# Optimization experiments

Measured on AMD Instinct MI355X. Metric: run time of the kernel, lower is better.

## Reference

```python
import jax, jax.numpy as jnp
import numpy as np

N_NODES = 50000
N_EDGES = 800000
NEG_SLOPE = 0.2  # DGL GATConv default LeakyReLU slope


def _gat_layer(h, src, dst, W, attn_l, attn_r, bias, activation):
    """One DGL-style GATConv (eval mode, no dropout).
    h: [N, Din]; W: [Din, H*F]; attn_l/attn_r: [H, F]; bias: [H*F].
    Returns [N, H, F].
    """
    H, F = attn_l.shape
    feat = (h @ W).reshape(-1, H, F)                      # [N, H, F]
    el = jnp.sum(feat * attn_l[None], axis=-1)            # [N, H]
    er = jnp.sum(feat * attn_r[None], axis=-1)            # [N, H]
    e = jax.nn.leaky_relu(el[src] + er[dst], NEG_SLOPE)   # [E, H]
    # segment softmax over incoming edges of each dst node
    m = jax.ops.segment_max(e, dst, num_segments=N_NODES)  # [N, H]
    ex = jnp.exp(e - m[dst])                               # [E, H]
    s = jax.ops.segment_sum(ex, dst, num_segments=N_NODES)  # [N, H]
    alpha = ex / s[dst]                                    # [E, H]
    msg = feat[src] * alpha[..., None]                     # [E, H, F]
    out = jax.ops.segment_sum(msg, dst, num_segments=N_NODES)  # [N, H, F]
    out = out + bias.reshape(1, H, F)
    if activation is not None:
        out = activation(out)
    return out


def setup_inputs() -> dict:
    key = jax.random.key(0)
    ks = jax.random.split(key, 16)
    in_size, hid, h0, h2, out_size = 256, 16, 8, 1, 64
    d1 = hid * h0  # 128
    inp = {
        "x": jax.random.normal(ks[0], (N_NODES, in_size), dtype=jnp.float32),
        "src": jax.random.randint(ks[1], (N_EDGES,), 0, N_NODES, dtype=jnp.int32),
        "dst": jax.random.randint(ks[2], (N_EDGES,), 0, N_NODES, dtype=jnp.int32),
        "W0": jax.random.normal(ks[3], (in_size, h0 * hid), dtype=jnp.float32) * 0.1,
        "al0": jax.random.normal(ks[4], (h0, hid), dtype=jnp.float32) * 0.1,
        "ar0": jax.random.normal(ks[5], (h0, hid), dtype=jnp.float32) * 0.1,
        "b0": jnp.zeros((h0 * hid,), dtype=jnp.float32),
        "W1": jax.random.normal(ks[6], (d1, h0 * hid), dtype=jnp.float32) * 0.1,
        "al1": jax.random.normal(ks[7], (h0, hid), dtype=jnp.float32) * 0.1,
        "ar1": jax.random.normal(ks[8], (h0, hid), dtype=jnp.float32) * 0.1,
        "b1": jnp.zeros((h0 * hid,), dtype=jnp.float32),
        "W2": jax.random.normal(ks[9], (d1, h2 * out_size), dtype=jnp.float32) * 0.1,
        "al2": jax.random.normal(ks[10], (h2, out_size), dtype=jnp.float32) * 0.1,
        "ar2": jax.random.normal(ks[11], (h2, out_size), dtype=jnp.float32) * 0.1,
        "b2": jnp.zeros((h2 * out_size,), dtype=jnp.float32),
    }
    return inp


def reference(x, src, dst, W0, al0, ar0, b0, W1, al1, ar1, b1, W2, al2, ar2, b2):
    elu = jax.nn.elu
    h = _gat_layer(x, src, dst, W0, al0, ar0, b0, elu)      # [N, 8, 16]
    h = h.reshape(h.shape[0], -1)                           # flatten heads -> [N, 128]
    h = _gat_layer(h, src, dst, W1, al1, ar1, b1, elu)      # [N, 8, 16]
    h = h.reshape(h.shape[0], -1)                           # [N, 128]
    h = _gat_layer(h, src, dst, W2, al2, ar2, b2, None)     # [N, 1, 64]
    return h.mean(axis=1)                                   # [N, 64]
```

## Files before the change

### kernel.cpp

```cpp
#include <hip/hip_runtime.h>
#include <hip/hip_bf16.h>
#include <hip/hip_fp16.h>
#include <cstdint>

#define N_NODES 50000
#define N_EDGES 800000

typedef _Float16 half8_t __attribute__((ext_vector_type(8)));
typedef float f32x4 __attribute__((ext_vector_type(4)));

template<int DIN, int DOUT, int F>
__device__ __forceinline__ void prepack_body(
    const float* __restrict__ W, const float* __restrict__ al,
    const float* __restrict__ ar, __half* __restrict__ Wp, int f)
{
    constexpr int NKS = DIN / 32;
    constexpr int NT  = DOUT / 16;
    constexpr int H   = DOUT / F;
    int lane = f & 63;
    int ks   = (f >> 6) % NKS;
    int nt   = (f >> 6) / NKS;
    int kbase = ks * 32 + (lane >> 4) * 8;
    int n = lane & 15;
    __half h[8];
    if (nt < NT) {
#pragma unroll
        for (int j = 0; j < 8; ++j)
            h[j] = __float2half(W[(size_t)(kbase + j) * DOUT + nt * 16 + n]);
    } else {
#pragma unroll
        for (int j = 0; j < 8; ++j) {
            float s = 0.f;
            if (n < H) {
                for (int ff = 0; ff < F; ++ff)
                    s += W[(size_t)(kbase + j) * DOUT + n * F + ff] * al[n * F + ff];
            } else if (n < 2 * H) {
                int hh = n - H;
                for (int ff = 0; ff < F; ++ff)
                    s += W[(size_t)(kbase + j) * DOUT + hh * F + ff] * ar[hh * F + ff];
            }
            h[j] = __float2half(s);
        }
    }
    *reinterpret_cast<uint4*>(&Wp[(size_t)f * 8]) = *reinterpret_cast<uint4*>(h);
}

__global__ void prepack_all(
    const float* __restrict__ W0, const float* __restrict__ al0, const float* __restrict__ ar0,
    const float* __restrict__ W1, const float* __restrict__ al1, const float* __restrict__ ar1,
    const float* __restrict__ W2, const float* __restrict__ al2, const float* __restrict__ ar2,
    __half* __restrict__ Wp0, __half* __restrict__ Wp1, __half* __restrict__ Wp2)
{
    int f = blockIdx.x * blockDim.x + threadIdx.x;
    if (f < 4608)       prepack_body<256, 128, 16>(W0, al0, ar0, Wp0, f);
    else if (f < 6912)  prepack_body<128, 128, 16>(W1, al1, ar1, Wp1, f - 4608);
    else if (f < 8192)  prepack_body<128, 64, 64>(W2, al2, ar2, Wp2, f - 6912);
}

template<int DIN, int DOUT, int F, typename XT>
__global__ __launch_bounds__(256) void gemm_attn_mfma(
    const XT* __restrict__ X, const __half* __restrict__ Wp,
    __half* __restrict__ feat, float* __restrict__ el, float* __restrict__ er, int N)
{
    constexpr int NKS = DIN / 32;
    constexpr int NT  = DOUT / 16;
    constexpr int NTT = NT + 1;
    constexpr int H   = DOUT / F;

    const int wid  = threadIdx.x >> 6;
    const int lane = threadIdx.x & 63;
    const int row0 = blockIdx.x * 64 + wid * 16;
    const int m    = lane & 15;
    const int kg   = lane >> 4;

    const int rowa = min(row0 + m, N - 1);
    const XT* Xr = X + (size_t)rowa * DIN + kg * 8;

    f32x4 acc[NTT];
#pragma unroll
    for (int i = 0; i < NTT; ++i) acc[i] = (f32x4){0.f, 0.f, 0.f, 0.f};

    if constexpr (sizeof(XT) == 4) {
        float4 xa = *reinterpret_cast<const float4*>(Xr);
        float4 xb = *reinterpret_cast<const float4*>(Xr + 4);
#pragma unroll
        for (int ks = 0; ks < NKS; ++ks) {
            float4 xan = xa, xbn = xb;
            if (ks + 1 < NKS) {
                xan = *reinterpret_cast<const float4*>(Xr + (ks + 1) * 32);
                xbn = *reinterpret_cast<const float4*>(Xr + (ks + 1) * 32 + 4);
            }
            half8_t a;
            a[0] = (_Float16)xa.x; a[1] = (_Float16)xa.y;
            a[2] = (_Float16)xa.z; a[3] = (_Float16)xa.w;
            a[4] = (_Float16)xb.x; a[5] = (_Float16)xb.y;
            a[6] = (_Float16)xb.z; a[7] = (_Float16)xb.w;
#pragma unroll
            for (int nt = 0; nt < NTT; ++nt) {
                const half8_t b = *reinterpret_cast<const half8_t*>(
                    Wp + ((size_t)(nt * NKS + ks) * 64 + lane) * 8);
                acc[nt] = __builtin_amdgcn_mfma_f32_16x16x32_f16(a, b, acc[nt], 0, 0, 0);
            }
            xa = xan; xb = xbn;
        }
    } else {
        half8_t a = *reinterpret_cast<const half8_t*>(Xr);
#pragma unroll
        for (int ks = 0; ks < NKS; ++ks) {
            half8_t an = a;
            if (ks + 1 < NKS)
                an = *reinterpret_cast<const half8_t*>(Xr + (ks + 1) * 32);
#pragma unroll
            for (int nt = 0; nt < NTT; ++nt) {
                const half8_t b = *reinterpret_cast<const half8_t*>(
                    Wp + ((size_t)(nt * NKS + ks) * 64 + lane) * 8);
                acc[nt] = __builtin_amdgcn_mfma_f32_16x16x32_f16(a, b, acc[nt], 0, 0, 0);
            }
            a = an;
        }
    }

    const int q = lane >> 4;
#pragma unroll
    for (int reg = 0; reg < 4; ++reg) {
        const int row = row0 + 4 * q + reg;
        if (row < N) {
#pragma unroll
            for (int nt = 0; nt < NT; ++nt)
                feat[(size_t)row * DOUT + nt * 16 + m] = __float2half(acc[nt][reg]);
            const float v = acc[NT][reg];
            if (m < H)          el[(size_t)row * H + m] = v;
            else if (m < 2 * H) er[(size_t)row * H + (m - H)] = v;
        }
    }
}

__global__ void zero_ints(int* __restrict__ a, int n)
{
    int i = blockIdx.x * blockDim.x + threadIdx.x;
    if (i < n) a[i] = 0;
}

__global__ __launch_bounds__(256) void hist_deg_part(
    const int* __restrict__ dst, int* __restrict__ deg)
{
    constexpr int RNG = N_NODES / 8;
    constexpr int SS  = N_EDGES / 100;
    const int g  = blockIdx.x & 7;
    const int s  = blockIdx.x >> 3;
    const int lo = g * RNG;
    const int e0 = s * SS;
    for (int q = threadIdx.x; q < SS / 4; q += 256) {
        const int4 d = *reinterpret_cast<const int4*>(&dst[e0 + 4 * q]);
#pragma unroll
        for (int k = 0; k < 4; ++k) {
            const int dv = (k == 0) ? d.x : (k == 1) ? d.y : (k == 2) ? d.z : d.w;
            if ((unsigned)(dv - lo) < (unsigned)RNG) atomicAdd(&deg[dv], 1);
        }
    }
}

__global__ __launch_bounds__(1024) void scan_partials(
    const int* __restrict__ deg, int* __restrict__ btot, int n)
{
    __shared__ int wsum[16];
    const int tid = threadIdx.x;
    const int lane = tid & 63, wid = tid >> 6;
    int i = blockIdx.x * 1024 + tid;
    int v = (i < n) ? deg[i] : 0;
#pragma unroll
    for (int off = 1; off < 64; off <<= 1) v += __shfl_xor(v, off);
    if (lane == 0) wsum[wid] = v;
    __syncthreads();
    if (tid < 16) {
        int w = wsum[tid];
#pragma unroll
        for (int off = 1; off < 16; off <<= 1) w += __shfl_xor(w, off, 16);
        if (tid == 0) btot[blockIdx.x] = w;
    }
}

__global__ void scan_btot(int* __restrict__ btot, int nb)
{
    int tid = threadIdx.x;
    int v = (tid < nb) ? btot[tid] : 0;
    int x = v;
#pragma unroll
    for (int off = 1; off < 64; off <<= 1) {
        int t = __shfl_up(x, off);
        if (tid >= off) x += t;
    }
    if (tid < nb) btot[tid] = x - v;
}

__global__ __launch_bounds__(1024) void scan_final(
    const int* __restrict__ deg, const int* __restrict__ bcar,
    int* __restrict__ offs, int* __restrict__ cursor, int n)
{
    __shared__ int wtot[16], wincl[16];
    const int tid = threadIdx.x;
    const int lane = tid & 63, wid = tid >> 6;
    int i = blockIdx.x * 1024 + tid;
    int v = (i < n) ? deg[i] : 0;
    int x = v;
#pragma unroll
    for (int off = 1; off < 64; off <<= 1) {
        int t = __shfl_up(x, off);
        if (lane >= off) x += t;
    }
    if (lane == 63) wtot[wid] = x;
    __syncthreads();
    if (tid < 16) {
        int wx = wtot[tid];
#pragma unroll
        for (int off = 1; off < 16; off <<= 1) {
            int t = __shfl_up(wx, off, 16);
            if (tid >= off) wx += t;
        }
        wincl[tid] = wx;
    }
    __syncthreads();
    int waveExcl = (wid == 0) ? 0 : wincl[wid - 1];
    if (i < n) {
        int o = bcar[blockIdx.x] + waveExcl + (x - v);
        offs[i] = o;
        cursor[i] = o;
    }
    if (i == 0) offs[n] = N_EDGES;
}

__global__ __launch_bounds__(256) void build_csr_part(
    const int* __restrict__ src, const int* __restrict__ dst,
    int* __restrict__ cursor, int* __restrict__ csr_src)
{
    constexpr int RNG = N_NODES / 8;
    constexpr int SS  = N_EDGES / 100;
    const int g  = blockIdx.x & 7;
    const int s  = blockIdx.x >> 3;
    const int lo = g * RNG;
    const int e0 = s * SS;

    for (int q = threadIdx.x; q < SS / 4; q += 256) {
        const int4 d = *reinterpret_cast<const int4*>(&dst[e0 + 4 * q]);
#pragma unroll
        for (int k = 0; k < 4; ++k) {
            const int dv = (k == 0) ? d.x : (k == 1) ? d.y : (k == 2) ? d.z : d.w;
            const unsigned r = (unsigned)(dv - lo);
            if (r < (unsigned)RNG) {
                int sv = src[e0 + 4 * q + k];
                int p = atomicAdd(&cursor[dv], 1);
                csr_src[p] = sv;
            }
        }
    }
}

template<int H, int F, bool ACT, typename OT>
__global__ __launch_bounds__(256) void node_flash_agg(
    const int* __restrict__ offs, const int* __restrict__ csr_src,
    const float* __restrict__ el, const float* __restrict__ er,
    const __half* __restrict__ feat, const float* __restrict__ bias,
    OT* __restrict__ out, int N)
{
    constexpr int D = H * F;
    constexpr int CPT = D / 64;
    constexpr int EPC = 64 / H;
    constexpr int MAXCH = (H == 8) ? 4 : 1;
    constexpr int SB = 8;
    constexpr int NB = MAXCH * EPC / SB;

    const int wid = threadIdx.x >> 6;
    const int lane = threadIdx.x & 63;
    const int n = blockIdx.x * 4 + wid;
    if (n >= N) return;

    const int beg = offs[n];
    const int deg = offs[n + 1] - beg;

    const int comp0 = CPT * lane;
    const int myhead = comp0 / F;

    auto store_out = [&](float a0, float a1) {
        if constexpr (CPT == 2) {
            if constexpr (sizeof(OT) == 2) {
                *reinterpret_cast<__half2*>(&out[(size_t)n * D + comp0]) =
                    __floats2half2_rn(a0, a1);
            } else {
                *reinterpret_cast<float2*>(&out[(size_t)n * D + comp0]) =
                    make_float2(a0, a1);
            }
        } else {
            out[(size_t)n * D + comp0] = (OT)a0;
        }
    };

    if (deg == 0) {
        float v0 = bias[comp0], v1 = (CPT == 2) ? bias[comp0 + 1] : 0.f;
        if (ACT) {
            v0 = (v0 > 0.f) ? v0 : (__expf(v0) - 1.f);
            v1 = (v1 > 0.f) ? v1 : (__expf(v1) - 1.f);
        }
        store_out(v0, v1);
        return;
    }

    const int h = lane % H;
    const int esub = lane / H;
    const float erd = er[(unsigned)(n * H) + h];

    float acc[CPT];
#pragma unroll
    for (int c = 0; c < CPT; ++c) acc[c] = 0.f;

    if (deg <= MAXCH * EPC) {
        const int nch = (deg + EPC - 1) / EPC;
        int sreg[MAXCH];
        float ex[MAXCH];

#pragma unroll
        for (int j = 0; j < MAXCH; ++j)
            if (j < nch)
                sreg[j] = csr_src[beg + min(j * EPC + esub, deg - 1)];

        if constexpr (CPT == 2) {
#pragma unroll
            for (int j = 0; j < MAXCH; ++j)
                if (j < nch) ex[j] = el[(unsigned)(sreg[j] * H) + h];

            unsigned fraw[MAXCH][EPC];
#pragma unroll
            for (int j = 0; j < MAXCH; ++j)
                if (j < nch)
#pragma unroll
                    for (int ii = 0; ii < EPC; ++ii) {
                        int sl = __shfl(sreg[j], ii * H);
                        fraw[j][ii] = *reinterpret_cast<const unsigned*>(
                            &feat[(unsigned)(sl * D) + comp0]);
                    }

            float m = -1e30f;
#pragma unroll
            for (int j = 0; j < MAXCH; ++j) {
                if (j < nch) {
                    float v = ex[j] + erd;
                    v = (v > 0.f) ? v : 0.2f * v;
                    v = (j * EPC + esub < deg) ? v : -1e30f;
                    ex[j] = v;
                    m = fmaxf(m, v);
                }
            }
#pragma unroll
            for (int off = H; off < 64; off <<= 1)
                m = fmaxf(m, __shfl_xor(m, off));
            float s = 0.f;
#pragma unroll
            for (int j = 0; j < MAXCH; ++j) {
                if (j < nch) { ex[j] = __expf(ex[j] - m); s += ex[j]; }
            }
#pragma unroll
            for (int off = H; off < 64; off <<= 1)
                s += __shfl_xor(s, off);
            const float inv = 1.f / s;
#pragma unroll
            for (int j = 0; j < MAXCH; ++j)
                if (j < nch) ex[j] *= inv;

#pragma unroll
            for (int j = 0; j < MAXCH; ++j) {
                if (j < nch) {
#pragma unroll
                    for (int ii = 0; ii < EPC; ++ii) {
                        float exb = __shfl(ex[j], ii * H + myhead);
                        __half2 h2;
                        *reinterpret_cast<unsigned*>(&h2) = fraw[j][ii];
                        const float2 f = __half22float2(h2);
                        acc[0] = fmaf(f.x, exb, acc[0]);
                        acc[1] = fmaf(f.y, exb, acc[1]);
                    }
                }
            }
        } else {
#pragma unroll
            for (int j = 0; j < MAXCH; ++j)
                if (j < nch) ex[j] = el[(unsigned)(sreg[j] * H) + h];
            float m = -1e30f;
#pragma unroll
            for (int j = 0; j < MAXCH; ++j) {
                if (j < nch) {
                    float v = ex[j] + erd;
                    v = (v > 0.f) ? v : 0.2f * v;
                    v = (j * EPC + esub < deg) ? v : -1e30f;
                    ex[j] = v;
                    m = fmaxf(m, v);
                }
            }
#pragma unroll
            for (int off = H; off < 64; off <<= 1)
                m = fmaxf(m, __shfl_xor(m, off));
            float s = 0.f;
#pragma unroll
            for (int j = 0; j < MAXCH; ++j) {
                if (j < nch) { ex[j] = __expf(ex[j] - m); s += ex[j]; }
            }
#pragma unroll
            for (int off = H; off < 64; off <<= 1)
                s += __shfl_xor(s, off);
            const float inv = 1.f / s;
#pragma unroll
            for (int j = 0; j < MAXCH; ++j)
                if (j < nch) ex[j] *= inv;

            float fvA[SB], fvB[SB];
            auto ldb = [&](int j, int g, float (&fv)[SB]) {
#pragma unroll
                for (int ii = 0; ii < SB; ++ii) {
                    int sl = __shfl(sreg[j], (g + ii) * H);
                    fv[ii] = __half2float(feat[(unsigned)(sl * D) + comp0]);
                }
            };
            auto fmab = [&](int j, int g, float (&fv)[SB]) {
#pragma unroll
                for (int ii = 0; ii < SB; ++ii) {
                    float exb = __shfl(ex[j], (g + ii) * H + myhead);
                    acc[0] = fmaf(fv[ii], exb, acc[0]);
                }
            };

            ldb(0, 0, fvA);
#pragma unroll
            for (int b = 0; b < NB; ++b) {
                if (b * SB < deg) {
                    if ((b + 1) * SB < deg) {
                        const int jn = ((b + 1) * SB) / EPC;
                        const int gn = ((b + 1) * SB) % EPC;
                        if ((b & 1) == 0) ldb(jn, gn, fvB);
                        else              ldb(jn, gn, fvA);
                    }
                    const int j = (b * SB) / EPC;
                    const int g = (b * SB) % EPC;
                    if ((b & 1) == 0) fmab(j, g, fvA);
                    else              fmab(j, g, fvB);
                }
            }
        }
#pragma unroll
        for (int c = 0; c < CPT; ++c) {
            float v = acc[c] + bias[comp0 + c];
            if (ACT) v = (v > 0.f) ? v : (__expf(v) - 1.f);
            acc[c] = v;
        }
    } else {
        float m_run = -1e30f, s_run = 0.f;
        int sN = csr_src[beg + min(esub, deg - 1)];
        float elN = el[(unsigned)(sN * H) + h];

        for (int base = 0; base < deg; base += EPC) {
            const int s_mine = sN;
            const float elv = elN;
            const int nb = base + EPC;
            if (nb < deg) {
                sN = csr_src[beg + min(nb + esub, deg - 1)];
                elN = el[(unsigned)(sN * H) + h];
            }
            float v = elv + erd;
            v = (v > 0.f) ? v : 0.2f * v;
            float logit = (base + esub < deg) ? v : -1e30f;

            float cmax = logit;
#pragma unroll
            for (int off = H; off < 64; off <<= 1)
                cmax = fmaxf(cmax, __shfl_xor(cmax, off));
            float nm = fmaxf(m_run, cmax);
            float scale = __expf(m_run - nm);
            float ex = __expf(logit - nm);
            float csum = ex;
#pragma unroll
            for (int off = H; off < 64; off <<= 1)
                csum += __shfl_xor(csum, off);
            s_run = s_run * scale + csum;
            m_run = nm;

            const float sc = __shfl(scale, myhead);
#pragma unroll
            for (int c = 0; c < CPT; ++c) acc[c] *= sc;

            const int active = min(EPC, deg - base);
            for (int g = 0; g < active; g += SB) {
                float fv[SB][CPT];
#pragma unroll
                for (int ii = 0; ii < SB; ++ii) {
                    int sl = __shfl(s_mine, (g + ii) * H);
                    if constexpr (CPT == 2) {
                        const __half2 t = *reinterpret_cast<const __half2*>(
                            &feat[(unsigned)(sl * D) + comp0]);
                        const float2 f = __half22float2(t);
                        fv[ii][0] = f.x; fv[ii][1] = f.y;
                    } else {
                        fv[ii][0] = __half2float(feat[(unsigned)(sl * D) + comp0]);
                    }
                }
#pragma unroll
                for (int ii = 0; ii < SB; ++ii) {
                    float exb = __shfl(ex, (g + ii) * H + myhead);
#pragma unroll
                    for (int c = 0; c < CPT; ++c)
                        acc[c] = fmaf(fv[ii][c], exb, acc[c]);
                }
            }
        }
        const float invb = __shfl(1.f / s_run, myhead);
#pragma unroll
        for (int c = 0; c < CPT; ++c) {
            float v = acc[c] * invb + bias[comp0 + c];
            if (ACT) v = (v > 0.f) ? v : (__expf(v) - 1.f);
            acc[c] = v;
        }
    }

    store_out(acc[0], (CPT == 2) ? acc[1] : 0.f);
}

extern "C" void kernel_launch(void* const* d_in, const int* in_sizes, int n_in,
                              void* d_out, int out_size, void* d_ws, size_t ws_size,
                              hipStream_t stream)
{
    const float* x   = (const float*)d_in[0];
    const int*   src = (const int*)d_in[1];
    const int*   dst = (const int*)d_in[2];
    const float* W0  = (const float*)d_in[3];
    const float* al0 = (const float*)d_in[4];
    const float* ar0 = (const float*)d_in[5];
    const float* b0  = (const float*)d_in[6];
    const float* W1  = (const float*)d_in[7];
    const float* al1 = (const float*)d_in[8];
    const float* ar1 = (const float*)d_in[9];
    const float* b1  = (const float*)d_in[10];
    const float* W2  = (const float*)d_in[11];
    const float* al2 = (const float*)d_in[12];
    const float* ar2 = (const float*)d_in[13];
    const float* b2  = (const float*)d_in[14];
    float* out = (float*)d_out;

    const int N = N_NODES, E = N_EDGES;

    const size_t wp0_h = 9 * 8 * 64 * 8;
    const size_t wp1_h = 9 * 4 * 64 * 8;
    const size_t wp2_h = 5 * 4 * 64 * 8;

    __half* Wp0 = (__half*)d_ws;
    __half* Wp1 = Wp0 + wp0_h;
    __half* Wp2 = Wp1 + wp1_h;
    float* fbase = (float*)(Wp2 + wp2_h + 2048);

    __half* feat  = (__half*)fbase;
    __half* hbufh = (__half*)(fbase + (size_t)N * 64);
    float* elb  = fbase + (size_t)N * 128;
    float* erb  = elb + (size_t)N * 8;
    int* ibase   = (int*)(erb + (size_t)N * 8);
    int* deg     = ibase;
    int* cursor  = deg + N;
    int* offs    = cursor + N;
    int* csr_src = offs + N + 1;
    int* btot    = csr_src + E;

    const int TB = 256;
    const int gb_rows64 = (N + 63) / 64;
    const int gb_nodes  = (N + 3) / 4;
    const int nsb       = (N + 1023) / 1024;

    prepack_all<<<32, 256, 0, stream>>>(W0, al0, ar0, W1, al1, ar1, W2, al2, ar2,
                                        Wp0, Wp1, Wp2);

    zero_ints<<<(N + TB - 1) / TB, TB, 0, stream>>>(deg, N);
    hist_deg_part<<<800, 256, 0, stream>>>(dst, deg);
    scan_partials<<<nsb, 1024, 0, stream>>>(deg, btot, N);
    scan_btot<<<1, 64, 0, stream>>>(btot, nsb);
    scan_final<<<nsb, 1024, 0, stream>>>(deg, btot, offs, cursor, N);
    build_csr_part<<<800, 256, 0, stream>>>(src, dst, cursor, csr_src);

    gemm_attn_mfma<256, 128, 16, float><<<gb_rows64, 256, 0, stream>>>(
        x, Wp0, feat, elb, erb, N);
    node_flash_agg<8, 16, true, __half><<<gb_nodes, 256, 0, stream>>>(
        offs, csr_src, elb, erb, feat, b0, hbufh, N);

    gemm_attn_mfma<128, 128, 16, __half><<<gb_rows64, 256, 0, stream>>>(
        hbufh, Wp1, feat, elb, erb, N);
    node_flash_agg<8, 16, true, __half><<<gb_nodes, 256, 0, stream>>>(
        offs, csr_src, elb, erb, feat, b1, hbufh, N);

    gemm_attn_mfma<128, 64, 64, __half><<<gb_rows64, 256, 0, stream>>>(
        hbufh, Wp2, feat, elb, erb, N);
    node_flash_agg<1, 64, false, float><<<gb_nodes, 256, 0, stream>>>(
        offs, csr_src, elb, erb, feat, b2, out, N);
}
```

Before: 262.3 us.

## Fuse degree zeroing into prepack and run layer-0 GEMM alongside CSR build

Folds the degree-array zeroing into the weight prepack kernel, and merges the layer-0 MFMA GEMM with the CSR scatter into one launch: the first 784 blocks do GEMM rows and the remaining 800 blocks build the CSR. This removes two kernel launches and lets the compute-bound GEMM overlap the atomic-heavy CSR build. The block count 782 is hardcoded for N=50000, and the GEMM now waits on the scan kernels even though it does not depend on them.

```diff
diff --git a/kernel.cpp b/kernel.cpp
--- a/kernel.cpp
+++ b/kernel.cpp
@@ -45,21 +45,26 @@
     *reinterpret_cast<uint4*>(&Wp[(size_t)f * 8]) = *reinterpret_cast<uint4*>(h);
 }
 
-__global__ void prepack_all(
+__global__ void prepack_zero(
     const float* __restrict__ W0, const float* __restrict__ al0, const float* __restrict__ ar0,
     const float* __restrict__ W1, const float* __restrict__ al1, const float* __restrict__ ar1,
     const float* __restrict__ W2, const float* __restrict__ al2, const float* __restrict__ ar2,
-    __half* __restrict__ Wp0, __half* __restrict__ Wp1, __half* __restrict__ Wp2)
+    __half* __restrict__ Wp0, __half* __restrict__ Wp1, __half* __restrict__ Wp2,
+    int* __restrict__ deg)
 {
     int f = blockIdx.x * blockDim.x + threadIdx.x;
     if (f < 4608)       prepack_body<256, 128, 16>(W0, al0, ar0, Wp0, f);
     else if (f < 6912)  prepack_body<128, 128, 16>(W1, al1, ar1, Wp1, f - 4608);
     else if (f < 8192)  prepack_body<128, 64, 64>(W2, al2, ar2, Wp2, f - 6912);
+    else {
+        int i = f - 8192;
+        if (i < N_NODES) deg[i] = 0;
+    }
 }
 
 template<int DIN, int DOUT, int F, typename XT>
-__global__ __launch_bounds__(256) void gemm_attn_mfma(
-    const XT* __restrict__ X, const __half* __restrict__ Wp,
+__device__ __forceinline__ void gemm_body(
+    int bid, const XT* __restrict__ X, const __half* __restrict__ Wp,
     __half* __restrict__ feat, float* __restrict__ el, float* __restrict__ er, int N)
 {
     constexpr int NKS = DIN / 32;
@@ -69,7 +74,7 @@
 
     const int wid  = threadIdx.x >> 6;
     const int lane = threadIdx.x & 63;
-    const int row0 = blockIdx.x * 64 + wid * 16;
+    const int row0 = bid * 64 + wid * 16;
     const int m    = lane & 15;
     const int kg   = lane >> 4;
 
@@ -135,10 +140,52 @@
     }
 }
 
-__global__ void zero_ints(int* __restrict__ a, int n)
-{
-    int i = blockIdx.x * blockDim.x + threadIdx.x;
-    if (i < n) a[i] = 0;
+template<int DIN, int DOUT, int F, typename XT>
+__global__ __launch_bounds__(256) void gemm_attn_mfma(
+    const XT* __restrict__ X, const __half* __restrict__ Wp,
+    __half* __restrict__ feat, float* __restrict__ el, float* __restrict__ er, int N)
+{
+    gemm_body<DIN, DOUT, F, XT>(blockIdx.x, X, Wp, feat, el, er, N);
+}
+
+__device__ __forceinline__ void build_body(
+    int bid, const int* __restrict__ src, const int* __restrict__ dst,
+    int* __restrict__ cursor, int* __restrict__ csr_src)
+{
+    constexpr int RNG = N_NODES / 8;
+    constexpr int SS  = N_EDGES / 100;
+    const int g  = bid & 7;
+    const int s  = bid >> 3;
+    const int lo = g * RNG;
+    const int e0 = s * SS;
+
+    for (int q = threadIdx.x; q < SS / 4; q += 256) {
+        const int4 d = *reinterpret_cast<const int4*>(&dst[e0 + 4 * q]);
+#pragma unroll
+        for (int k = 0; k < 4; ++k) {
+            const int dv = (k == 0) ? d.x : (k == 1) ? d.y : (k == 2) ? d.z : d.w;
+            const unsigned r = (unsigned)(dv - lo);
+            if (r < (unsigned)RNG) {
+                int sv = src[e0 + 4 * q + k];
+                int p = atomicAdd(&cursor[dv], 1);
+                csr_src[p] = sv;
+            }
+        }
+    }
+}
+
+__global__ __launch_bounds__(256) void gemm0_csr(
+    const float* __restrict__ X, const __half* __restrict__ Wp0,
+    __half* __restrict__ feat, float* __restrict__ el, float* __restrict__ er, int N,
+    const int* __restrict__ src, const int* __restrict__ dst,
+    int* __restrict__ cursor, int* __restrict__ csr_src)
+{
+    if (blockIdx.x < 784) {
+        if (blockIdx.x < 782)
+            gemm_body<256, 128, 16, float>(blockIdx.x, X, Wp0, feat, el, er, N);
+    } else {
+        build_body(blockIdx.x - 784, src, dst, cursor, csr_src);
+    }
 }
 
 __global__ __launch_bounds__(256) void hist_deg_part(
@@ -227,32 +274,6 @@
         cursor[i] = o;
     }
     if (i == 0) offs[n] = N_EDGES;
-}
-
-__global__ __launch_bounds__(256) void build_csr_part(
-    const int* __restrict__ src, const int* __restrict__ dst,
-    int* __restrict__ cursor, int* __restrict__ csr_src)
-{
-    constexpr int RNG = N_NODES / 8;
-    constexpr int SS  = N_EDGES / 100;
-    const int g  = blockIdx.x & 7;
-    const int s  = blockIdx.x >> 3;
-    const int lo = g * RNG;
-    const int e0 = s * SS;
-
-    for (int q = threadIdx.x; q < SS / 4; q += 256) {
-        const int4 d = *reinterpret_cast<const int4*>(&dst[e0 + 4 * q]);
-#pragma unroll
-        for (int k = 0; k < 4; ++k) {
-            const int dv = (k == 0) ? d.x : (k == 1) ? d.y : (k == 2) ? d.z : d.w;
-            const unsigned r = (unsigned)(dv - lo);
-            if (r < (unsigned)RNG) {
-                int sv = src[e0 + 4 * q + k];
-                int p = atomicAdd(&cursor[dv], 1);
-                csr_src[p] = sv;
-            }
-        }
-    }
 }
 
 template<int H, int F, bool ACT, typename OT>
@@ -563,23 +584,22 @@
     int* csr_src = offs + N + 1;
     int* btot    = csr_src + E;
 
-    const int TB = 256;
     const int gb_rows64 = (N + 63) / 64;
     const int gb_nodes  = (N + 3) / 4;
     const int nsb       = (N + 1023) / 1024;
-
-    prepack_all<<<32, 256, 0, stream>>>(W0, al0, ar0, W1, al1, ar1, W2, al2, ar2,
-                                        Wp0, Wp1, Wp2);
-
-    zero_ints<<<(N + TB - 1) / TB, TB, 0, stream>>>(deg, N);
+    const int gb_pz     = (8192 + N + 255) / 256;
+
+    prepack_zero<<<gb_pz, 256, 0, stream>>>(W0, al0, ar0, W1, al1, ar1, W2, al2, ar2,
+                                            Wp0, Wp1, Wp2, deg);
+
     hist_deg_part<<<800, 256, 0, stream>>>(dst, deg);
     scan_partials<<<nsb, 1024, 0, stream>>>(deg, btot, N);
     scan_btot<<<1, 64, 0, stream>>>(btot, nsb);
     scan_final<<<nsb, 1024, 0, stream>>>(deg, btot, offs, cursor, N);
-    build_csr_part<<<800, 256, 0, stream>>>(src, dst, cursor, csr_src);
-
-    gemm_attn_mfma<256, 128, 16, float><<<gb_rows64, 256, 0, stream>>>(
-        x, Wp0, feat, elb, erb, N);
+
+    gemm0_csr<<<784 + 800, 256, 0, stream>>>(x, Wp0, feat, elb, erb, N,
+                                             src, dst, cursor, csr_src);
+
     node_flash_agg<8, 16, true, __half><<<gb_nodes, 256, 0, stream>>>(
         offs, csr_src, elb, erb, feat, b0, hbufh, N);
 
```

New measurement: 261.0 us. Within noise of the previous version (-0.5%).
